# Kernel tuning notes

Hardware: AMD Instinct MI355X
Metric: run time of the kernel (lower is better)

The kernel has to match this reference:

```python
import jax, jax.numpy as jnp
import numpy as np

VALUE_SCALE = 0.1  # paper: values ~ N(0, (0.1*std)^2); weights are unit-std here


def setup_inputs() -> dict:
    key = jax.random.key(0)
    k1, k2, k3, k4 = jax.random.split(key, 4)
    O, I = 4096, 4096
    n_flip = 1_000_000
    x = jax.random.normal(k1, (256, I), dtype=jnp.float32)
    weight = jax.random.normal(k2, (O, I), dtype=jnp.float32)
    prune_mask = jax.random.uniform(k3, (O, I)) < 0.6
    weight = jnp.where(prune_mask, 0.0, weight)
    flip_idx = jax.random.randint(k4, (n_flip,), 0, O * I, dtype=jnp.int64)
    values = jax.random.normal(jax.random.fold_in(key, 7), (n_flip,), dtype=jnp.float32)
    return {"x": x, "weight": weight, "flip_idx": flip_idx, "values": values}


def reference(x, weight, flip_idx, values):
    # 'restore' mode: scatter small random values into pruned weight positions
    # (single fused scatter instead of a python loop of scalar writes),
    # then run the wrapped model's forward (Linear without bias).
    O, I = weight.shape
    w_flat = weight.reshape(-1)
    w_mod = w_flat.at[flip_idx].set(values * VALUE_SCALE).reshape(O, I)
    # y = x @ W^T  -- [B, I] x [O, I] -> [B, O]
    return jnp.einsum('bi,oi->bo', x, w_mod)
```

## Files before the change

### kernel.cpp

```cpp
#include <hip/hip_runtime.h>
#include <hip/hip_bf16.h>
#include <stdint.h>
#include <stddef.h>

#define BATCH 256
#define OC 4096
#define IC 4096
#define VALUE_SCALE 0.1f

#define BN 64
#define BK 32
#define KS 8
#define KPER (IC / KS)
#define NT (KPER / BK)
#define YSZ (BATCH * OC)

typedef float f32x4 __attribute__((ext_vector_type(4)));
typedef int   i32x4 __attribute__((ext_vector_type(4)));
typedef short bf16x8 __attribute__((ext_vector_type(8)));

__device__ __forceinline__ short f2bf(float f) {
    return (short)__bfloat16_as_ushort(__float2bfloat16(f));
}

__global__ void scatter_k(float* __restrict__ w, const int* __restrict__ idx,
                          const float* __restrict__ val, int n) {
    int i = (blockIdx.x * blockDim.x + threadIdx.x) * 4;
    if (i + 4 <= n) {
        i32x4 id = *(const i32x4*)(idx + i);
        f32x4 v  = *(const f32x4*)(val + i);
        w[id[0]] = v[0] * VALUE_SCALE;
        w[id[1]] = v[1] * VALUE_SCALE;
        w[id[2]] = v[2] * VALUE_SCALE;
        w[id[3]] = v[3] * VALUE_SCALE;
    } else {
        for (int j = i; j < n; ++j) w[idx[j]] = val[j] * VALUE_SCALE;
    }
}

__global__ __launch_bounds__(256, 2) void gemm_k(const float* __restrict__ x,
                                                 const float* __restrict__ w,
                                                 float* __restrict__ part,
                                                 float* __restrict__ y) {
    const int tid  = threadIdx.x;
    const int lane = tid & 63;
    const int wv   = tid >> 6;
    const int bid  = blockIdx.x;
    const int ks   = bid & 7;
    const int bn   = bid >> 3;
    const int k0   = ks * KPER;
    const int nc0  = bn * BN;

    const int r = lane & 15;
    const int q = lane >> 4;

    const float* xbase = x + (size_t)(wv * 64 + r) * IC + k0 + q * 8;
    const float* wbase = w + (size_t)(nc0 + r)     * IC + k0 + q * 8;

    f32x4 acc[4][4];
#pragma unroll
    for (int m = 0; m < 4; ++m)
#pragma unroll
        for (int n = 0; n < 4; ++n) acc[m][n] = (f32x4)0.0f;

    f32x4 ra[8], rb[8];
    bf16x8 fa[4], fb[4];

    auto loadRaw = [&](int t) {
        const int ko = t * BK;
#pragma unroll
        for (int m = 0; m < 4; ++m) {
            const float* s = xbase + (size_t)m * 16 * IC + ko;
            ra[2 * m]     = *(const f32x4*)s;
            ra[2 * m + 1] = *(const f32x4*)(s + 4);
        }
#pragma unroll
        for (int n = 0; n < 4; ++n) {
            const float* s = wbase + (size_t)n * 16 * IC + ko;
            rb[2 * n]     = *(const f32x4*)s;
            rb[2 * n + 1] = *(const f32x4*)(s + 4);
        }
    };

    auto cvtAll = [&]() {
#pragma unroll
        for (int m = 0; m < 4; ++m) {
#pragma unroll
            for (int j = 0; j < 4; ++j) {
                fa[m][j]     = f2bf(ra[2 * m][j]);
                fa[m][j + 4] = f2bf(ra[2 * m + 1][j]);
                fb[m][j]     = f2bf(rb[2 * m][j]);
                fb[m][j + 4] = f2bf(rb[2 * m + 1][j]);
            }
        }
    };

    loadRaw(0);
    for (int t = 0; t < NT; ++t) {
        cvtAll();
        if (t + 1 < NT) loadRaw(t + 1);
#pragma unroll
        for (int n = 0; n < 4; ++n)
#pragma unroll
            for (int m = 0; m < 4; ++m)
                acc[m][n] = __builtin_amdgcn_mfma_f32_16x16x32_bf16(fa[m], fb[n], acc[m][n], 0, 0, 0);
    }

    if (part) {
        float* dst = part + (size_t)ks * YSZ;
#pragma unroll
        for (int m = 0; m < 4; ++m) {
            int r0 = wv * 64 + m * 16 + (lane >> 4) * 4;
#pragma unroll
            for (int n = 0; n < 4; ++n) {
                int c = nc0 + n * 16 + (lane & 15);
#pragma unroll
                for (int rr = 0; rr < 4; ++rr)
                    dst[(size_t)(r0 + rr) * OC + c] = acc[m][n][rr];
            }
        }
    } else {
#pragma unroll
        for (int m = 0; m < 4; ++m) {
            int r0 = wv * 64 + m * 16 + (lane >> 4) * 4;
#pragma unroll
            for (int n = 0; n < 4; ++n) {
                int c = nc0 + n * 16 + (lane & 15);
#pragma unroll
                for (int rr = 0; rr < 4; ++rr)
                    atomicAdd(&y[(size_t)(r0 + rr) * OC + c], acc[m][n][rr]);
            }
        }
    }
}

__global__ void reduce_k(const float* __restrict__ part, float* __restrict__ y) {
    int i = (blockIdx.x * blockDim.x + threadIdx.x) * 4;
    f32x4 s = *(const f32x4*)(part + i);
#pragma unroll
    for (int p = 1; p < KS; ++p) s += *(const f32x4*)(part + (size_t)p * YSZ + i);
    *(f32x4*)(y + i) = s;
}

extern "C" void kernel_launch(void* const* d_in, const int* in_sizes, int n_in,
                              void* d_out, int out_size, void* d_ws, size_t ws_size,
                              hipStream_t stream) {
    const float* x  = (const float*)d_in[0];
    float*       w  = (float*)d_in[1];
    const int*   fi = (const int*)d_in[2];
    const float* fv = (const float*)d_in[3];
    float*       y  = (float*)d_out;
    const int nflip = in_sizes[2];

    const bool use_ws = ws_size >= (size_t)KS * YSZ * sizeof(float);
    float* part = use_ws ? (float*)d_ws : nullptr;

    if (!use_ws) hipMemsetAsync(d_out, 0, (size_t)out_size * sizeof(float), stream);
    scatter_k<<<dim3((nflip + 1023) / 1024), dim3(256), 0, stream>>>(w, fi, fv, nflip);
    gemm_k<<<dim3((OC / BN) * KS), dim3(256), 0, stream>>>(x, w, part, y);
    if (use_ws)
        reduce_k<<<dim3(YSZ / (4 * 256)), dim3(256), 0, stream>>>(part, y);
}
```

Baseline: 173.2 us.

## Stage bf16 tiles through double-buffered swizzled LDS with 512-thread blocks

The GEMM kernel now converts x and W tiles to bf16 once per block and stores them in double-buffered, XOR-swizzled shared memory instead of having every wave load and convert its own fp32 fragments from global memory. Blocks grow to 8 waves, each owning 32 rows, with barriers separating the LDS write and compute phases. This is meant to cut redundant global loads and conversions of the W tile across waves and raise occupancy. In exchange it adds LDS traffic and two barriers per K step, and each wave does less MFMA work between syncs.

```diff
diff --git a/kernel.cpp b/kernel.cpp
--- a/kernel.cpp
+++ b/kernel.cpp
@@ -23,6 +23,13 @@
     return (short)__bfloat16_as_ushort(__float2bfloat16(f));
 }
 
+__device__ __forceinline__ void barrier_nodrain() {
+    asm volatile("s_waitcnt lgkmcnt(0)" ::: "memory");
+    __builtin_amdgcn_sched_barrier(0);
+    __builtin_amdgcn_s_barrier();
+    __builtin_amdgcn_sched_barrier(0);
+}
+
 __global__ void scatter_k(float* __restrict__ w, const int* __restrict__ idx,
                           const float* __restrict__ val, int n) {
     int i = (blockIdx.x * blockDim.x + threadIdx.x) * 4;
@@ -38,7 +45,7 @@
     }
 }
 
-__global__ __launch_bounds__(256, 2) void gemm_k(const float* __restrict__ x,
+__global__ __launch_bounds__(512, 4) void gemm_k(const float* __restrict__ x,
                                                  const float* __restrict__ w,
                                                  float* __restrict__ part,
                                                  float* __restrict__ y) {
@@ -51,66 +58,91 @@
     const int k0   = ks * KPER;
     const int nc0  = bn * BN;
 
-    const int r = lane & 15;
-    const int q = lane >> 4;
+    __shared__ __align__(16) short At[2][BATCH * BK];
+    __shared__ __align__(16) short Bt[2][BN * BK];
 
-    const float* xbase = x + (size_t)(wv * 64 + r) * IC + k0 + q * 8;
-    const float* wbase = w + (size_t)(nc0 + r)     * IC + k0 + q * 8;
-
-    f32x4 acc[4][4];
+    f32x4 acc[2][4];
 #pragma unroll
-    for (int m = 0; m < 4; ++m)
+    for (int m = 0; m < 2; ++m)
 #pragma unroll
         for (int n = 0; n < 4; ++n) acc[m][n] = (f32x4)0.0f;
 
-    f32x4 ra[8], rb[8];
-    bf16x8 fa[4], fb[4];
+    const int arow = tid >> 1, ah = tid & 1;
+    const int brow = tid >> 2, bq = tid & 3;
 
-    auto loadRaw = [&](int t) {
-        const int ko = t * BK;
+    f32x4 ra[4], rb[2];
+
+    auto load_regs = [&](int t) {
+        const float* s = x + (size_t)arow * IC + k0 + t * BK + ah * 16;
+        ra[0] = *(const f32x4*)s;
+        ra[1] = *(const f32x4*)(s + 4);
+        ra[2] = *(const f32x4*)(s + 8);
+        ra[3] = *(const f32x4*)(s + 12);
+        if (tid < 256) {
+            const float* sb = w + (size_t)(nc0 + brow) * IC + k0 + t * BK + bq * 8;
+            rb[0] = *(const f32x4*)sb;
+            rb[1] = *(const f32x4*)(sb + 4);
+        }
+    };
+
+    auto write_lds = [&](int buf) {
+        const int swa = (arow >> 1) & 3;
+        bf16x8 v0, v1;
 #pragma unroll
-        for (int m = 0; m < 4; ++m) {
-            const float* s = xbase + (size_t)m * 16 * IC + ko;
-            ra[2 * m]     = *(const f32x4*)s;
-            ra[2 * m + 1] = *(const f32x4*)(s + 4);
+        for (int q = 0; q < 4; ++q) {
+            v0[q] = f2bf(ra[0][q]); v0[q + 4] = f2bf(ra[1][q]);
+            v1[q] = f2bf(ra[2][q]); v1[q + 4] = f2bf(ra[3][q]);
+        }
+        *(bf16x8*)&At[buf][arow * BK + ((2 * ah)     ^ swa) * 8] = v0;
+        *(bf16x8*)&At[buf][arow * BK + ((2 * ah + 1) ^ swa) * 8] = v1;
+        if (tid < 256) {
+            bf16x8 vb;
+#pragma unroll
+            for (int q = 0; q < 4; ++q) { vb[q] = f2bf(rb[0][q]); vb[q + 4] = f2bf(rb[1][q]); }
+            *(bf16x8*)&Bt[buf][brow * BK + (bq ^ ((brow >> 1) & 3)) * 8] = vb;
+        }
+    };
+
+    auto compute = [&](int buf) {
+        const int fr = lane & 15, cs = lane >> 4;
+        bf16x8 a[2], b[4];
+#pragma unroll
+        for (int m = 0; m < 2; ++m) {
+            int row = wv * 32 + m * 16 + fr;
+            a[m] = *(const bf16x8*)&At[buf][row * BK + ((cs ^ ((row >> 1) & 3))) * 8];
         }
 #pragma unroll
         for (int n = 0; n < 4; ++n) {
-            const float* s = wbase + (size_t)n * 16 * IC + ko;
-            rb[2 * n]     = *(const f32x4*)s;
-            rb[2 * n + 1] = *(const f32x4*)(s + 4);
+            int row = n * 16 + fr;
+            b[n] = *(const bf16x8*)&Bt[buf][row * BK + ((cs ^ ((row >> 1) & 3))) * 8];
         }
-    };
-
-    auto cvtAll = [&]() {
-#pragma unroll
-        for (int m = 0; m < 4; ++m) {
-#pragma unroll
-            for (int j = 0; j < 4; ++j) {
-                fa[m][j]     = f2bf(ra[2 * m][j]);
-                fa[m][j + 4] = f2bf(ra[2 * m + 1][j]);
-                fb[m][j]     = f2bf(rb[2 * m][j]);
-                fb[m][j + 4] = f2bf(rb[2 * m + 1][j]);
-            }
-        }
-    };
-
-    loadRaw(0);
-    for (int t = 0; t < NT; ++t) {
-        cvtAll();
-        if (t + 1 < NT) loadRaw(t + 1);
 #pragma unroll
         for (int n = 0; n < 4; ++n)
 #pragma unroll
-            for (int m = 0; m < 4; ++m)
-                acc[m][n] = __builtin_amdgcn_mfma_f32_16x16x32_bf16(fa[m], fb[n], acc[m][n], 0, 0, 0);
+            for (int m = 0; m < 2; ++m)
+                acc[m][n] = __builtin_amdgcn_mfma_f32_16x16x32_bf16(a[m], b[n], acc[m][n], 0, 0, 0);
+    };
+
+    load_regs(0);
+    write_lds(0);
+    barrier_nodrain();
+
+    for (int t = 0; t < NT; ++t) {
+        const int cur = t & 1;
+        if (t + 1 < NT) load_regs(t + 1);
+        compute(cur);
+        barrier_nodrain();
+        if (t + 1 < NT) {
+            write_lds(cur ^ 1);
+            barrier_nodrain();
+        }
     }
 
     if (part) {
         float* dst = part + (size_t)ks * YSZ;
 #pragma unroll
-        for (int m = 0; m < 4; ++m) {
-            int r0 = wv * 64 + m * 16 + (lane >> 4) * 4;
+        for (int m = 0; m < 2; ++m) {
+            int r0 = wv * 32 + m * 16 + (lane >> 4) * 4;
 #pragma unroll
             for (int n = 0; n < 4; ++n) {
                 int c = nc0 + n * 16 + (lane & 15);
@@ -121,8 +153,8 @@
         }
     } else {
 #pragma unroll
-        for (int m = 0; m < 4; ++m) {
-            int r0 = wv * 64 + m * 16 + (lane >> 4) * 4;
+        for (int m = 0; m < 2; ++m) {
+            int r0 = wv * 32 + m * 16 + (lane >> 4) * 4;
 #pragma unroll
             for (int n = 0; n < 4; ++n) {
                 int c = nc0 + n * 16 + (lane & 15);
@@ -157,7 +189,7 @@
 
     if (!use_ws) hipMemsetAsync(d_out, 0, (size_t)out_size * sizeof(float), stream);
     scatter_k<<<dim3((nflip + 1023) / 1024), dim3(256), 0, stream>>>(w, fi, fv, nflip);
-    gemm_k<<<dim3((OC / BN) * KS), dim3(256), 0, stream>>>(x, w, part, y);
+    gemm_k<<<dim3((OC / BN) * KS), dim3(512), 0, stream>>>(x, w, part, y);
     if (use_ws)
         reduce_k<<<dim3(YSZ / (4 * 256)), dim3(256), 0, stream>>>(part, y);
 }
```

Result: faster. 151.8 us (-12.3%).
